# Kernel optimization log

Hardware: AMD Instinct MI355X
Metric: run time of the kernel (lower is better)

## Reference

```python
import jax, jax.numpy as jnp
import numpy as np

SEARCH_RANGE = 4


def _cost_volume(x1, x2):
    """PWC-Net style windowed shift-correlation cost volume.

    x1, x2: [B, H, W, C] (channels-last).
    Returns [B, H, W, (2*sr+1)**2], normalized by H (matches original,
    which divides by shape[1]). Channel index is (D*i + j) mod D*D to
    replicate torch's negative-index wraparound in the original code.
    """
    sr = SEARCH_RANGE
    D = 2 * sr + 1
    B, H, W, C = x1.shape
    # Zero-pad x2 so out-of-range shifts contribute 0 (matches zeros-init cv).
    x2p = jnp.pad(x2, ((0, 0), (sr, sr), (sr, sr), (0, 0)))
    outs = [None] * (D * D)
    for i in range(-sr, sr + 1):
        for j in range(-sr, sr + 1):
            idx = (D * i + j) % (D * D)  # torch negative-index wrap
            # x1 row h pairs with x2 row h - i (col w with w - j)
            shifted = jax.lax.dynamic_slice(x2p, (0, sr - i, sr - j, 0), (B, H, W, C))
            outs[idx] = jnp.sum(x1 * shifted, axis=-1)  # [B, H, W]
    cv = jnp.stack(outs, axis=-1)  # [B, H, W, D*D]
    return cv / H


def setup_inputs() -> dict:
    key = jax.random.key(0)
    k1, k2 = jax.random.split(key)
    B, H, W, C = 8, 128, 128, 128
    x1 = jax.random.normal(k1, (B, H, W, C), dtype=jnp.float32)
    x2 = jax.random.normal(k2, (B, H, W, C), dtype=jnp.float32)
    return {"x1": x1, "x2": x2}


def reference(x1, x2):
    return _cost_volume(x1, x2)
```

## Files before the change

kernel.cpp:

```cpp
#include <hip/hip_runtime.h>

#define SR 4
#define DD 9
#define NIDX 81
#define HH 128
#define WW 128
#define CC 128
#define ROWS 4
#define COLS 136
#define PPX 8
#define CHUNKC 32
#define NCH (CC / CHUNKC)
#define C4S (CHUNKC / 4)
#define LDS_F4 (ROWS * COLS * C4S)

__global__ __launch_bounds__(256, 2)
void cost_volume_kernel(const float* __restrict__ x1,
                        const float* __restrict__ x2,
                        float* __restrict__ out) {
    __shared__ float4 x2s4[LDS_F4];
    float* x2s = (float*)x2s4;

    const int tid  = threadIdx.x;
    const int wave = tid >> 6;
    const int lane = tid & 63;
    const int gl   = lane & 15;
    const int q    = lane >> 4;

    const int b    = blockIdx.x >> 5;
    const int h0   = (blockIdx.x & 31) * ROWS;
    const int half = blockIdx.y;

    const int row = wave;
    const int w0  = gl * PPX;

    const float* x1p = x1 + ((size_t)((b * HH + h0 + row) * WW + w0)) * CC;
    const float* x2b = x2 + (size_t)b * HH * WW * CC;
    float* outp = out + ((size_t)((b * HH + h0 + row) * WW)) * NIDX;

    const int c4w      = tid & (C4S - 1);
    const int stage_hi = tid >> 3;

    const int i_lo = half ? 1 : -SR;
    const int i_hi = half ? SR : 0;

    for (int i = i_lo; i <= i_hi; ++i) {
        float acc[PPX][DD];
        #pragma unroll
        for (int p = 0; p < PPX; ++p)
            #pragma unroll
            for (int j = 0; j < DD; ++j) acc[p][j] = 0.f;

        for (int ch = 0; ch < NCH; ++ch) {
            const int cbase = ch * CHUNKC;
            __syncthreads();
            for (int k = 0; k < 17; ++k) {
                int tmp = stage_hi + (k << 5);
                int r   = tmp / COLS;
                int ps  = tmp - r * COLS;
                int hp  = h0 + r - i;
                int wp  = ps - SR;
                float4 v = make_float4(0.f, 0.f, 0.f, 0.f);
                if ((unsigned)hp < (unsigned)HH && (unsigned)wp < (unsigned)WW)
                    v = *(const float4*)(x2b + (size_t)(hp * WW + wp) * CC + cbase + 4 * c4w);
                int slot4 = tmp * C4S + (c4w ^ ((ps >> 3) & 7));
                x2s4[slot4] = v;
            }
            __syncthreads();
            #pragma unroll
            for (int t = 0; t < 2; ++t) {
                const int cl  = 16 * t + 4 * q;
                const int c4v = 4 * t + q;

                float4 a[PPX];
                #pragma unroll
                for (int p = 0; p < PPX; ++p)
                    a[p] = *(const float4*)(x1p + p * CC + cbase + cl);

                float4 v[16];
                #pragma unroll
                for (int d = 0; d < 16; ++d) {
                    int ps    = w0 + d;
                    int slot4 = (row * COLS + ps) * C4S + (c4v ^ ((ps >> 3) & 7));
                    v[d] = x2s4[slot4];
                }

                #pragma unroll
                for (int p = 0; p < PPX; ++p) {
                    #pragma unroll
                    for (int j = 0; j < DD; ++j) {
                        const float4 xv = v[p + 8 - j];
                        float s = acc[p][j];
                        s = fmaf(a[p].x, xv.x, s);
                        s = fmaf(a[p].y, xv.y, s);
                        s = fmaf(a[p].z, xv.z, s);
                        s = fmaf(a[p].w, xv.w, s);
                        acc[p][j] = s;
                    }
                }
            }
        }

        #pragma unroll
        for (int p = 0; p < PPX; ++p) {
            #pragma unroll
            for (int j = 0; j < DD; ++j) {
                float s = acc[p][j];
                s += __shfl_xor(s, 16, 64);
                s += __shfl_xor(s, 32, 64);
                acc[p][j] = s;
            }
        }

        const float inv = 1.0f / (float)HH;
        #pragma unroll
        for (int p = 0; p < PPX; ++p) {
            if ((p >> 1) == q) {
                float* op = outp + (size_t)(w0 + p) * NIDX;
                #pragma unroll
                for (int j = 0; j < DD; ++j) {
                    int idx = 9 * i + (j - SR);
                    if (idx < 0) idx += NIDX;
                    op[idx] = acc[p][j] * inv;
                }
            }
        }
    }
}

extern "C" void kernel_launch(void* const* d_in, const int* in_sizes, int n_in,
                              void* d_out, int out_size, void* d_ws, size_t ws_size,
                              hipStream_t stream) {
    const float* x1 = (const float*)d_in[0];
    const float* x2 = (const float*)d_in[1];
    float* out = (float*)d_out;
    (void)in_sizes; (void)n_in; (void)out_size; (void)d_ws; (void)ws_size;

    dim3 grid(256, 2);
    dim3 block(256);
    hipLaunchKernelGGL(cost_volume_kernel, grid, block, 0, stream, x1, x2, out);
}
```

Before: 682.3 us.

## Stage cost volume in scratch and transpose to output via separate LDS kernel

The main kernel writes each shift row's 9 correlations contiguously into a workspace buffer instead of scattering them at 81-float stride into the output. A second kernel gathers the 9 row-shift slabs through shared memory and writes fully coalesced output rows with the torch-style index wraparound. This targets uncoalesced strided stores but adds a full extra round trip of the cost volume through global memory and a second launch. It falls back to direct stores when the workspace is too small.

```diff
diff --git a/kernel.cpp b/kernel.cpp
--- a/kernel.cpp
+++ b/kernel.cpp
@@ -14,10 +14,14 @@
 #define C4S (CHUNKC / 4)
 #define LDS_F4 (ROWS * COLS * C4S)
 
+#define SCRATCH_FLOATS ((size_t)8 * 9 * HH * WW * DD)
+#define SCRATCH_BYTES  (SCRATCH_FLOATS * 4)
+
+template <bool DIRECT>
 __global__ __launch_bounds__(256, 2)
 void cost_volume_kernel(const float* __restrict__ x1,
                         const float* __restrict__ x2,
-                        float* __restrict__ out) {
+                        float* __restrict__ dst) {
     __shared__ float4 x2s4[LDS_F4];
     float* x2s = (float*)x2s4;
 
@@ -36,7 +40,6 @@
 
     const float* x1p = x1 + ((size_t)((b * HH + h0 + row) * WW + w0)) * CC;
     const float* x2b = x2 + (size_t)b * HH * WW * CC;
-    float* outp = out + ((size_t)((b * HH + h0 + row) * WW)) * NIDX;
 
     const int c4w      = tid & (C4S - 1);
     const int stage_hi = tid >> 3;
@@ -113,18 +116,65 @@
         }
 
         const float inv = 1.0f / (float)HH;
-        #pragma unroll
-        for (int p = 0; p < PPX; ++p) {
-            if ((p >> 1) == q) {
-                float* op = outp + (size_t)(w0 + p) * NIDX;
-                #pragma unroll
-                for (int j = 0; j < DD; ++j) {
-                    int idx = 9 * i + (j - SR);
-                    if (idx < 0) idx += NIDX;
-                    op[idx] = acc[p][j] * inv;
+        if (DIRECT) {
+            float* outp = dst + ((size_t)((b * HH + h0 + row) * WW)) * NIDX;
+            #pragma unroll
+            for (int p = 0; p < PPX; ++p) {
+                if ((p >> 1) == q) {
+                    float* op = outp + (size_t)(w0 + p) * NIDX;
+                    #pragma unroll
+                    for (int j = 0; j < DD; ++j) {
+                        int idx = 9 * i + (j - SR);
+                        if (idx < 0) idx += NIDX;
+                        op[idx] = acc[p][j] * inv;
+                    }
+                }
+            }
+        } else {
+            const size_t rbase = (((size_t)(b * 9 + (i + 4)) * HH + (h0 + row)) * WW) * DD;
+            #pragma unroll
+            for (int p = 0; p < PPX; ++p) {
+                if ((p >> 1) == q) {
+                    float* sp = dst + rbase + (size_t)(w0 + p) * DD;
+                    #pragma unroll
+                    for (int j = 0; j < DD; ++j)
+                        sp[j] = acc[p][j] * inv;
                 }
             }
         }
+    }
+}
+
+__global__ __launch_bounds__(256)
+void cv_transpose(const float* __restrict__ ws, float* __restrict__ out) {
+    __shared__ float lds[32 * NIDX];
+
+    const int blk = blockIdx.x;
+    const int wc  = blk & 3;
+    const int h   = (blk >> 2) & 127;
+    const int b   = blk >> 9;
+
+    const float* sb = ws + (size_t)b * 9 * HH * WW * DD + (size_t)h * WW * DD + wc * 32 * DD;
+
+    for (int k = 0; k < 11; ++k) {
+        int e = threadIdx.x + (k << 8);
+        if (e < 9 * 288) {
+            int il = e / 288;
+            int r  = e - 288 * il;
+            float v = sb[(size_t)il * (HH * WW * DD) + r];
+            int j  = r % 9;
+            int wl = r / 9;
+            int n  = 9 * il + j - 40;
+            if (n < 0) n += NIDX;
+            lds[wl * NIDX + n] = v;
+        }
+    }
+    __syncthreads();
+
+    float* ob = out + ((size_t)(b * HH + h) * WW + wc * 32) * NIDX;
+    for (int k = 0; k < 11; ++k) {
+        int e = threadIdx.x + (k << 8);
+        if (e < 32 * NIDX) ob[e] = lds[e];
     }
 }
 
@@ -134,9 +184,16 @@
     const float* x1 = (const float*)d_in[0];
     const float* x2 = (const float*)d_in[1];
     float* out = (float*)d_out;
-    (void)in_sizes; (void)n_in; (void)out_size; (void)d_ws; (void)ws_size;
+    (void)in_sizes; (void)n_in; (void)out_size;
 
     dim3 grid(256, 2);
     dim3 block(256);
-    hipLaunchKernelGGL(cost_volume_kernel, grid, block, 0, stream, x1, x2, out);
+
+    if (d_ws != nullptr && ws_size >= SCRATCH_BYTES) {
+        float* scratch = (float*)d_ws;
+        hipLaunchKernelGGL((cost_volume_kernel<false>), grid, block, 0, stream, x1, x2, scratch);
+        hipLaunchKernelGGL(cv_transpose, dim3(4096), block, 0, stream, scratch, out);
+    } else {
+        hipLaunchKernelGGL((cost_volume_kernel<true>), grid, block, 0, stream, x1, x2, out);
+    }
 }
```

Result: slower. 794.9 us (+16.5%).

## Double-buffer x2 staging via async global-to-LDS loads with scratch transpose output

Applied to the files above, without the earlier changes.

Replaces the synchronous register-staged x2 tile load with double-buffered 16-channel chunks loaded through global_load_lds. Out-of-range halo cells read from a zeroed workspace buffer. The x1 loads for the next phase are prefetched so that loads overlap compute. When enough workspace is available, results go to a shift-major scratch layout with coalesced float2 stores, and a second kernel transposes them into the 81-channel output. This adds a memset, an extra kernel launch and a full round trip of the output through scratch memory. A legacy path is kept as a fallback.

```diff
diff --git a/kernel.cpp b/kernel.cpp
--- a/kernel.cpp
+++ b/kernel.cpp
@@ -1,4 +1,5 @@
 #include <hip/hip_runtime.h>
+#include <stdint.h>
 
 #define SR 4
 #define DD 9
@@ -7,102 +8,260 @@
 #define WW 128
 #define CC 128
 #define ROWS 4
-#define COLS 136
-#define PPX 8
-#define CHUNKC 32
-#define NCH (CC / CHUNKC)
-#define C4S (CHUNKC / 4)
-#define LDS_F4 (ROWS * COLS * C4S)
-
+#define CELLS 144
+#define CHUNKC 16
+#define C4S 4
+#define ROW_F4 (CELLS * C4S)
+#define BUF_F4 (ROWS * ROW_F4)
+#define ZBYTES 4096
+#define SCR_OFF 4096
+#define SCR_FLOATS ((size_t)8 * 9 * HH * WW * DD)
+#define SCR_BYTES (SCR_FLOATS * 4)
+
+__device__ __forceinline__ void gload16(const void* g, void* l) {
+    __builtin_amdgcn_global_load_lds(
+        (const __attribute__((address_space(1))) void*)g,
+        (__attribute__((address_space(3))) void*)l, 16, 0, 0);
+}
+
+#define ST18(A, B, g2)                         \
+    do {                                       \
+        g2[0] = make_float2(A[0], A[1]);       \
+        g2[1] = make_float2(A[2], A[3]);       \
+        g2[2] = make_float2(A[4], A[5]);       \
+        g2[3] = make_float2(A[6], A[7]);       \
+        g2[4] = make_float2(A[8], B[0]);       \
+        g2[5] = make_float2(B[1], B[2]);       \
+        g2[6] = make_float2(B[3], B[4]);       \
+        g2[7] = make_float2(B[5], B[6]);       \
+        g2[8] = make_float2(B[7], B[8]);       \
+    } while (0)
+
+template <bool SCRATCH>
 __global__ __launch_bounds__(256, 2)
-void cost_volume_kernel(const float* __restrict__ x1,
-                        const float* __restrict__ x2,
-                        float* __restrict__ out) {
-    __shared__ float4 x2s4[LDS_F4];
-    float* x2s = (float*)x2s4;
+void cv_main(const float* __restrict__ x1, const float* __restrict__ x2,
+             const float* __restrict__ zbuf, float* __restrict__ dst) {
+    __shared__ float4 buf[2][BUF_F4];
 
     const int tid  = threadIdx.x;
-    const int wave = tid >> 6;
+    const int wv   = tid >> 6;
     const int lane = tid & 63;
     const int gl   = lane & 15;
     const int q    = lane >> 4;
+    const int w0   = gl * 8;
 
     const int b    = blockIdx.x >> 5;
     const int h0   = (blockIdx.x & 31) * ROWS;
     const int half = blockIdx.y;
-
-    const int row = wave;
-    const int w0  = gl * PPX;
-
+    const int i_lo = half ? 1 : -SR;
+    const int nph  = (half ? 4 : 5) * 8;
+
+    const float* x1p = x1 + ((size_t)((b * HH + h0 + wv) * WW + w0)) * CC;
+    const char*  x2c = (const char*)(x2 + (size_t)b * HH * WW * CC);
+
+    float  acc[8][DD];
+    float4 a0[8], a1[8];
+
+    auto stage = [&](int ph, int tb) {
+        const int i  = i_lo + (ph >> 3);
+        const int cb = (ph & 7) * CHUNKC;
+        const int hp = h0 + wv - i;
+        const bool rowok = (unsigned)hp < (unsigned)HH;
+        const char* rowg = x2c + (size_t)hp * (WW * CC * 4) + cb * 4;
+        float4* drow = &buf[tb][wv * ROW_F4];
+        #pragma unroll
+        for (int k = 0; k < 9; ++k) {
+            const int slot = 16 * k + (lane >> 2);
+            const int sh   = 2 * k + (lane >> 5);
+            const int ps   = slot ^ (sh & 7);
+            const int c4   = (lane & 3) ^ (sh & 3);
+            const int wp   = ps - SR;
+            const void* g = (rowok && (unsigned)wp < (unsigned)WW)
+                          ? (const void*)(rowg + wp * 512 + c4 * 16)
+                          : (const void*)((const char*)zbuf + ((64 * k + lane) & 255) * 16);
+            gload16(g, (void*)(drow + 64 * k));
+        }
+    };
+
+    auto ldx1 = [&](int ph, float4* a) {
+        const int cb = (ph & 7) * CHUNKC;
+        #pragma unroll
+        for (int p = 0; p < 8; ++p)
+            a[p] = *(const float4*)(x1p + (size_t)p * CC + cb + 4 * q);
+    };
+
+    auto compute = [&](int tb, const float4* a) {
+        const float4* src = &buf[tb][wv * ROW_F4];
+        float4 v[16];
+        #pragma unroll
+        for (int d = 0; d < 16; ++d) {
+            const int ps = w0 + d;
+            const int sh = ps >> 3;
+            v[d] = src[(ps ^ (sh & 7)) * 4 + (q ^ (sh & 3))];
+        }
+        #pragma unroll
+        for (int p = 0; p < 8; ++p) {
+            #pragma unroll
+            for (int j = 0; j < DD; ++j) {
+                const float4 xv = v[p + 8 - j];
+                float s = acc[p][j];
+                s = fmaf(a[p].x, xv.x, s);
+                s = fmaf(a[p].y, xv.y, s);
+                s = fmaf(a[p].z, xv.z, s);
+                s = fmaf(a[p].w, xv.w, s);
+                acc[p][j] = s;
+            }
+        }
+    };
+
+    auto flush = [&](int ph) {
+        const int i = i_lo + (ph >> 3);
+        #pragma unroll
+        for (int p = 0; p < 8; ++p) {
+            #pragma unroll
+            for (int j = 0; j < DD; ++j) {
+                float s = acc[p][j];
+                s += __shfl_xor(s, 16, 64);
+                s += __shfl_xor(s, 32, 64);
+                acc[p][j] = s * (1.0f / (float)HH);
+            }
+        }
+        if (SCRATCH) {
+            const size_t rbase = (((size_t)(b * 9 + (i + 4)) * HH + (h0 + wv)) * WW) * DD;
+            float2* g2 = (float2*)(dst + rbase + (size_t)w0 * DD + 18 * q);
+            if      (q == 0) ST18(acc[0], acc[1], g2);
+            else if (q == 1) ST18(acc[2], acc[3], g2);
+            else if (q == 2) ST18(acc[4], acc[5], g2);
+            else             ST18(acc[6], acc[7], g2);
+        } else {
+            float* outp = dst + ((size_t)((b * HH + h0 + wv) * WW)) * NIDX;
+            #pragma unroll
+            for (int p = 0; p < 8; ++p) {
+                if ((p >> 1) == q) {
+                    float* op = outp + (size_t)(w0 + p) * NIDX;
+                    #pragma unroll
+                    for (int j = 0; j < DD; ++j) {
+                        int idx = 9 * i + (j - SR);
+                        if (idx < 0) idx += NIDX;
+                        op[idx] = acc[p][j];
+                    }
+                }
+            }
+        }
+        #pragma unroll
+        for (int p = 0; p < 8; ++p)
+            #pragma unroll
+            for (int j = 0; j < DD; ++j) acc[p][j] = 0.f;
+    };
+
+    #pragma unroll
+    for (int p = 0; p < 8; ++p)
+        #pragma unroll
+        for (int j = 0; j < DD; ++j) acc[p][j] = 0.f;
+
+    stage(0, 0);
+    ldx1(0, a0);
+    __syncthreads();
+
+    for (int ph = 0; ph < nph; ph += 2) {
+        stage(ph + 1, 1);
+        ldx1(ph + 1, a1);
+        compute(0, a0);
+        __syncthreads();
+        if (ph + 2 < nph) { stage(ph + 2, 0); ldx1(ph + 2, a0); }
+        compute(1, a1);
+        if (((ph + 1) & 7) == 7) flush(ph + 1);
+        __syncthreads();
+    }
+}
+
+__global__ __launch_bounds__(288)
+void cv_transpose(const float* __restrict__ ws, float* __restrict__ out) {
+    __shared__ float lds[32 * NIDX];
+    const int t   = threadIdx.x;
+    const int blk = blockIdx.x;
+    const int wc  = blk & 3;
+    const int h   = (blk >> 2) & 127;
+    const int b   = blk >> 9;
+    const int wl  = t / 9;
+    const int j   = t - 9 * wl;
+
+    const float* sb = ws + (size_t)b * 9 * (HH * WW * DD)
+                         + (size_t)h * (WW * DD) + wc * (32 * DD) + t;
+    #pragma unroll
+    for (int il = 0; il < 9; ++il) {
+        float v = sb[(size_t)il * (HH * WW * DD)];
+        int n = 9 * il + j - 40;
+        if (n < 0) n += NIDX;
+        lds[wl * NIDX + n] = v;
+    }
+    __syncthreads();
+    float* ob = out + ((size_t)(b * HH + h) * WW + wc * 32) * NIDX;
+    #pragma unroll
+    for (int k = 0; k < 9; ++k) ob[t + 288 * k] = lds[t + 288 * k];
+}
+
+#define LCOLS 136
+#define LC4S 8
+#define LLDS_F4 (ROWS * LCOLS * LC4S)
+__global__ __launch_bounds__(256, 2)
+void cv_legacy(const float* __restrict__ x1, const float* __restrict__ x2,
+               float* __restrict__ out) {
+    __shared__ float4 x2s4[LLDS_F4];
+    const int tid = threadIdx.x, wave = tid >> 6, lane = tid & 63;
+    const int gl = lane & 15, q = lane >> 4;
+    const int b = blockIdx.x >> 5, h0 = (blockIdx.x & 31) * ROWS, half = blockIdx.y;
+    const int row = wave, w0 = gl * 8;
     const float* x1p = x1 + ((size_t)((b * HH + h0 + row) * WW + w0)) * CC;
     const float* x2b = x2 + (size_t)b * HH * WW * CC;
-    float* outp = out + ((size_t)((b * HH + h0 + row) * WW)) * NIDX;
-
-    const int c4w      = tid & (C4S - 1);
-    const int stage_hi = tid >> 3;
-
-    const int i_lo = half ? 1 : -SR;
-    const int i_hi = half ? SR : 0;
-
+    const int c4w = tid & 7, shi = tid >> 3;
+    const int i_lo = half ? 1 : -SR, i_hi = half ? SR : 0;
     for (int i = i_lo; i <= i_hi; ++i) {
-        float acc[PPX][DD];
-        #pragma unroll
-        for (int p = 0; p < PPX; ++p)
+        float acc[8][DD];
+        #pragma unroll
+        for (int p = 0; p < 8; ++p)
             #pragma unroll
             for (int j = 0; j < DD; ++j) acc[p][j] = 0.f;
-
-        for (int ch = 0; ch < NCH; ++ch) {
-            const int cbase = ch * CHUNKC;
+        for (int ch = 0; ch < 4; ++ch) {
+            const int cbase = ch * 32;
             __syncthreads();
             for (int k = 0; k < 17; ++k) {
-                int tmp = stage_hi + (k << 5);
-                int r   = tmp / COLS;
-                int ps  = tmp - r * COLS;
-                int hp  = h0 + r - i;
-                int wp  = ps - SR;
+                int tmp = shi + (k << 5);
+                int r = tmp / LCOLS, ps = tmp - r * LCOLS;
+                int hp = h0 + r - i, wp = ps - SR;
                 float4 v = make_float4(0.f, 0.f, 0.f, 0.f);
                 if ((unsigned)hp < (unsigned)HH && (unsigned)wp < (unsigned)WW)
                     v = *(const float4*)(x2b + (size_t)(hp * WW + wp) * CC + cbase + 4 * c4w);
-                int slot4 = tmp * C4S + (c4w ^ ((ps >> 3) & 7));
-                x2s4[slot4] = v;
+                x2s4[tmp * LC4S + (c4w ^ ((ps >> 3) & 7))] = v;
             }
             __syncthreads();
             #pragma unroll
             for (int t = 0; t < 2; ++t) {
-                const int cl  = 16 * t + 4 * q;
-                const int c4v = 4 * t + q;
-
-                float4 a[PPX];
+                const int cl = 16 * t + 4 * q, c4v = 4 * t + q;
+                float4 a[8];
                 #pragma unroll
-                for (int p = 0; p < PPX; ++p)
+                for (int p = 0; p < 8; ++p)
                     a[p] = *(const float4*)(x1p + p * CC + cbase + cl);
-
                 float4 v[16];
                 #pragma unroll
                 for (int d = 0; d < 16; ++d) {
-                    int ps    = w0 + d;
-                    int slot4 = (row * COLS + ps) * C4S + (c4v ^ ((ps >> 3) & 7));
-                    v[d] = x2s4[slot4];
+                    int ps = w0 + d;
+                    v[d] = x2s4[(row * LCOLS + ps) * LC4S + (c4v ^ ((ps >> 3) & 7))];
                 }
-
                 #pragma unroll
-                for (int p = 0; p < PPX; ++p) {
+                for (int p = 0; p < 8; ++p)
                     #pragma unroll
                     for (int j = 0; j < DD; ++j) {
                         const float4 xv = v[p + 8 - j];
                         float s = acc[p][j];
-                        s = fmaf(a[p].x, xv.x, s);
-                        s = fmaf(a[p].y, xv.y, s);
-                        s = fmaf(a[p].z, xv.z, s);
-                        s = fmaf(a[p].w, xv.w, s);
+                        s = fmaf(a[p].x, xv.x, s); s = fmaf(a[p].y, xv.y, s);
+                        s = fmaf(a[p].z, xv.z, s); s = fmaf(a[p].w, xv.w, s);
                         acc[p][j] = s;
                     }
-                }
-            }
-        }
-
-        #pragma unroll
-        for (int p = 0; p < PPX; ++p) {
+            }
+        }
+        #pragma unroll
+        for (int p = 0; p < 8; ++p)
             #pragma unroll
             for (int j = 0; j < DD; ++j) {
                 float s = acc[p][j];
@@ -110,11 +269,10 @@
                 s += __shfl_xor(s, 32, 64);
                 acc[p][j] = s;
             }
-        }
-
         const float inv = 1.0f / (float)HH;
-        #pragma unroll
-        for (int p = 0; p < PPX; ++p) {
+        float* outp = out + ((size_t)((b * HH + h0 + row) * WW)) * NIDX;
+        #pragma unroll
+        for (int p = 0; p < 8; ++p)
             if ((p >> 1) == q) {
                 float* op = outp + (size_t)(w0 + p) * NIDX;
                 #pragma unroll
@@ -124,7 +282,6 @@
                     op[idx] = acc[p][j] * inv;
                 }
             }
-        }
     }
 }
 
@@ -134,9 +291,20 @@
     const float* x1 = (const float*)d_in[0];
     const float* x2 = (const float*)d_in[1];
     float* out = (float*)d_out;
-    (void)in_sizes; (void)n_in; (void)out_size; (void)d_ws; (void)ws_size;
-
+    (void)in_sizes; (void)n_in; (void)out_size;
+
+    dim3 block(256);
     dim3 grid(256, 2);
-    dim3 block(256);
-    hipLaunchKernelGGL(cost_volume_kernel, grid, block, 0, stream, x1, x2, out);
-}
+
+    if (d_ws != nullptr && ws_size >= SCR_OFF + SCR_BYTES) {
+        hipMemsetAsync(d_ws, 0, ZBYTES, stream);
+        float* scr = (float*)((char*)d_ws + SCR_OFF);
+        cv_main<true><<<grid, block, 0, stream>>>(x1, x2, (const float*)d_ws, scr);
+        cv_transpose<<<dim3(4096), dim3(288), 0, stream>>>(scr, out);
+    } else if (d_ws != nullptr && ws_size >= ZBYTES) {
+        hipMemsetAsync(d_ws, 0, ZBYTES, stream);
+        cv_main<false><<<grid, block, 0, stream>>>(x1, x2, (const float*)d_ws, out);
+    } else {
+        cv_legacy<<<grid, block, 0, stream>>>(x1, x2, out);
+    }
+}
```

Result: slower. 710.5 us (+4.1%).
